# Performance work log

Measured on AMD Instinct MI355X. Metric: run time of the kernel, lower is better.

Reference implementation:

```python
import jax, jax.numpy as jnp
import numpy as np


def _conv_bn_relu(x, w, g, b):
    # 1x1 conv over channel dim + BatchNorm(eval, affine) + ReLU; x: [B,Cin,...]
    y = jnp.einsum('oc,bc...->bo...', w, x)
    shp = (1, -1) + (1,) * (y.ndim - 2)
    return jax.nn.relu(y * g.reshape(shp) + b.reshape(shp))


def _gather(feat, idx):
    # feat [B,d,N], idx [B,M] -> [B,d,M]  (torch.gather along dim 2)
    return jnp.take_along_axis(feat, idx[:, None, :], axis=2)


def _lfa(f, neigh_idx, w, g, b):
    # Local Feature Aggregation: gather k neighbors, concat with center, 1x1 conv, max over k.
    Bn, Np, k = neigh_idx.shape
    fs = f[..., 0]                                   # [B,d,N]
    d = fs.shape[1]
    neigh = _gather(fs, neigh_idx.reshape(Bn, Np * k)).reshape(Bn, d, Np, k)
    cat = jnp.concatenate([jnp.broadcast_to(f, neigh.shape), neigh], axis=1)  # [B,2d,N,k]
    return _conv_bn_relu(cat, w, g, b).max(axis=3, keepdims=True)             # [B,d_out,N,1]


def _random_sample(f, pool_idx):
    # f [B,d,N,1], pool_idx [B,N',k] -> [B,d,N',1] via gather + max over k
    Bn, Np, k = pool_idx.shape
    fs = f[..., 0]
    d = fs.shape[1]
    gth = _gather(fs, pool_idx.reshape(Bn, Np * k)).reshape(Bn, d, Np, k)
    return gth.max(axis=3, keepdims=True)


def _interp(f, interp_idx):
    # f [B,d,N,1], interp_idx [B,M,1] -> [B,d,M,1] nearest-neighbor upsample
    Bn, M, _ = interp_idx.shape
    return _gather(f[..., 0], interp_idx.reshape(Bn, M))[..., None]


def setup_inputs() -> dict:
    key = jax.random.key(0)
    B, K = 2, 16
    Ns = (16384, 4096, 1024, 256, 64)
    ks = list(jax.random.split(key, 64))
    ki = iter(ks)
    inp = {}
    inp['xyz'] = jax.random.normal(next(ki), (B, Ns[0], 3), jnp.float32)
    for i in range(4):
        inp['neigh%d' % i] = jax.random.randint(next(ki), (B, Ns[i], K), 0, Ns[i], jnp.int32)
        inp['pool%d' % i] = jax.random.randint(next(ki), (B, Ns[i + 1], K), 0, Ns[i], jnp.int32)
        inp['up%d' % i] = jax.random.randint(next(ki), (B, Ns[i], 1), 0, Ns[i + 1], jnp.int32)

    def mk(name, co, cin):
        inp[name + '_w'] = jax.random.normal(next(ki), (co, cin), jnp.float32) * 0.02
        inp[name + '_g'] = jnp.ones((co,), jnp.float32)
        inp[name + '_b'] = jnp.zeros((co,), jnp.float32)

    mk('fc0', 64, 3)
    mk('l1', 128, 128)
    mk('l2', 256, 256)
    mk('l3', 512, 512)
    mk('l4', 1024, 1024)
    mk('dt', 1024, 1024)
    mk('d4', 512, 2048)
    mk('d3', 256, 1024)
    mk('d2', 128, 512)
    mk('d1', 64, 256)
    mk('d0', 64, 64)
    return inp


def reference(xyz, neigh0, neigh1, neigh2, neigh3, pool0, pool1, pool2, pool3, up0, up1, up2, up3, fc0_w, fc0_g, fc0_b, l1_w, l1_g, l1_b, l2_w, l2_g, l2_b, l3_w, l3_g, l3_b, l4_w, l4_g, l4_b, dt_w, dt_g, dt_b, d4_w, d4_g, d4_b, d3_w, d3_g, d3_b, d2_w, d2_g, d2_b, d1_w, d1_g, d1_b, d0_w, d0_g, d0_b):
    out0 = _conv_bn_relu(jnp.transpose(xyz, (0, 2, 1)), fc0_w, fc0_g, fc0_b)[..., None]  # [B,64,N0,1]
    out1 = _lfa(out0, neigh0, l1_w, l1_g, l1_b)        # [B,128,N0,1]
    out1p = _random_sample(out1, pool0)                # [B,128,N1,1]
    out2 = _lfa(out1p, neigh1, l2_w, l2_g, l2_b)       # [B,256,N1,1]
    out2p = _random_sample(out2, pool1)                # [B,256,N2,1]
    out3 = _lfa(out2p, neigh2, l3_w, l3_g, l3_b)       # [B,512,N2,1]
    out3p = _random_sample(out3, pool2)                # [B,512,N3,1]
    out4 = _lfa(out3p, neigh3, l4_w, l4_g, l4_b)       # [B,1024,N3,1]
    out4p = _random_sample(out4, pool3)                # [B,1024,N4,1]
    out = _conv_bn_relu(out4p, dt_w, dt_g, dt_b)
    out = _conv_bn_relu(jnp.concatenate([out, out4p], 1), d4_w, d4_g, d4_b)
    out = _interp(out, up3)
    out = _conv_bn_relu(jnp.concatenate([out, out3p], 1), d3_w, d3_g, d3_b)
    out = _interp(out, up2)
    out = _conv_bn_relu(jnp.concatenate([out, out2p], 1), d2_w, d2_g, d2_b)
    out = _interp(out, up1)
    out = _conv_bn_relu(jnp.concatenate([out, out1p], 1), d1_w, d1_g, d1_b)
    out = _interp(out, up0)
    out = _conv_bn_relu(out, d0_w, d0_g, d0_b)         # [B,out_d,N0,1]
    return out
```

## Files before the change

### kernel.cpp

```cpp
#include <hip/hip_runtime.h>

typedef unsigned short u16;
typedef unsigned int u32;
typedef short s16x8 __attribute__((ext_vector_type(8)));
typedef float f32x4 __attribute__((ext_vector_type(4)));

__device__ __forceinline__ float bf2f(u16 u) {
  union { u32 i; float f; } c;
  c.i = ((u32)u) << 16;
  return c.f;
}
__device__ __forceinline__ u16 f2bf(float f) {
  union { float f; u32 i; } c;
  c.f = f;
  u32 r = c.i + 0x7FFFu + ((c.i >> 16) & 1u);
  return (u16)(r >> 16);
}
__device__ __forceinline__ float rbf(float x) {
  union { float f; u32 u; } c;
  c.f = x;
  u32 r = c.u + 0x7FFFu + ((c.u >> 16) & 1u);
  c.u = (r >> 16) << 16;
  return c.f;
}
__device__ __forceinline__ float ldin(const void* p, size_t i, int isBf) {
  if (isBf) return bf2f(((const u16*)p)[i]);
  return rbf(((const float*)p)[i]);
}
__device__ __forceinline__ void ld4bf(const u16* p, float* v) {
  uint2 q = *reinterpret_cast<const uint2*>(p);
  v[0] = bf2f((u16)(q.x & 0xFFFFu));
  v[1] = bf2f((u16)(q.x >> 16));
  v[2] = bf2f((u16)(q.y & 0xFFFFu));
  v[3] = bf2f((u16)(q.y >> 16));
}
__device__ __forceinline__ void st4bf(u16* p, const float* v) {
  uint2 q;
  q.x = (u32)f2bf(v[0]) | (((u32)f2bf(v[1])) << 16);
  q.y = (u32)f2bf(v[2]) | (((u32)f2bf(v[3])) << 16);
  *reinterpret_cast<uint2*>(p) = q;
}

__global__ void C3Dnet_34600256537193_kernel() {}

__global__ void probe_kernel(const u16* x, int* flag) {
  if (threadIdx.x == 0 && blockIdx.x == 0) {
    int sane = 0;
    for (int i = 0; i < 256; i += 2) {
      int e = (x[i] >> 7) & 0xFF;
      if (e >= 97 && e <= 137) ++sane;
    }
    *flag = (sane >= 64) ? 1 : 0;
  }
}

__global__ __launch_bounds__(256) void sentinel_kernel(u16* out, int n, float v) {
  u16 u = f2bf(v);
  int i0 = (blockIdx.x * 256 + threadIdx.x) * 8;
  for (int j = 0; j < 8; ++j)
    if (i0 + j < n) out[i0 + j] = u;
}

__global__ __launch_bounds__(256) void cvt_kernel(
    const void* s0, const void* s1, const void* s2, const void* s3, const void* s4,
    const void* s5, const void* s6, const void* s7, const void* s8, const void* s9,
    u16* dst, const int* dtF) {
  const int f = *dtF;
  int blk = blockIdx.x;
  const void* src;
  int base, boff;
  if (blk < 8)         { src = s0; base = 0;       boff = 0;    }
  else if (blk < 40)   { src = s1; base = 16384;   boff = 8;    }
  else if (blk < 168)  { src = s2; base = 81920;   boff = 40;   }
  else if (blk < 680)  { src = s3; base = 344064;  boff = 168;  }
  else if (blk < 1192) { src = s4; base = 1392640; boff = 680;  }
  else if (blk < 1704) { src = s5; base = 2441216; boff = 1192; }
  else if (blk < 1832) { src = s6; base = 3489792; boff = 1704; }
  else if (blk < 1864) { src = s7; base = 3751936; boff = 1832; }
  else if (blk < 1872) { src = s8; base = 3817472; boff = 1864; }
  else                 { src = s9; base = 3833856; boff = 1872; }
  int local = (blk - boff) * 2048 + (int)threadIdx.x * 8;
  u16* dp = dst + base + local;
  if (f) {
    *reinterpret_cast<uint4*>(dp) =
        *reinterpret_cast<const uint4*>((const u16*)src + local);
  } else {
    const float4* sp = reinterpret_cast<const float4*>((const float*)src + local);
    float4 a = sp[0], b = sp[1];
    uint4 o;
    o.x = (u32)f2bf(a.x) | (((u32)f2bf(a.y)) << 16);
    o.y = (u32)f2bf(a.z) | (((u32)f2bf(a.w)) << 16);
    o.z = (u32)f2bf(b.x) | (((u32)f2bf(b.y)) << 16);
    o.w = (u32)f2bf(b.z) | (((u32)f2bf(b.w)) << 16);
    *reinterpret_cast<uint4*>(dp) = o;
  }
}

__global__ __launch_bounds__(256) void fc0_kernel(
    const void* xyz, const void* w, const void* g, const void* be,
    u16* out, int N, const int* dtF) {
  int f = *dtF;
  int o = threadIdx.x & 63;
  int n = blockIdx.x * 4 + (threadIdx.x >> 6);
  int b = blockIdx.y;
  if (n >= N) return;
  size_t pb = ((size_t)b * N + n) * 3;
  float acc = ldin(w, o * 3 + 0, f) * ldin(xyz, pb + 0, f) +
              ldin(w, o * 3 + 1, f) * ldin(xyz, pb + 1, f) +
              ldin(w, o * 3 + 2, f) * ldin(xyz, pb + 2, f);
  acc = acc * ldin(g, o, f) + ldin(be, o, f);
  if (acc < 0.0f) acc = 0.0f;
  out[((size_t)b * N + n) * 64 + o] = f2bf(acc);
}

__global__ __launch_bounds__(256) void gather_max_kernel(
    const void* src, int srcBf16, int srcStride, int srcOff, int Nsrc,
    const void* cen, int cenBf16, int cenStride,
    const int* idx, void* out, int outBf16, int Np, int C, int doRelu) {
  int c4n = C >> 2;
  int ptsPerBlk = 256 / c4n;
  int p = (int)threadIdx.x / c4n;
  int c4 = (int)threadIdx.x % c4n;
  int n = blockIdx.x * ptsPerBlk + p;
  int b = blockIdx.y;
  if (n >= Np) return;
  const int* ip = idx + ((size_t)b * Np + n) * 16;
  float m[4];
  m[0] = m[1] = m[2] = m[3] = -3.0e38f;
  for (int k = 0; k < 16; ++k) {
    size_t base = ((size_t)b * Nsrc + ip[k]) * srcStride + srcOff + (c4 << 2);
    float v[4];
    if (srcBf16) {
      ld4bf((const u16*)src + base, v);
    } else {
      float4 t = *reinterpret_cast<const float4*>((const float*)src + base);
      v[0] = t.x; v[1] = t.y; v[2] = t.z; v[3] = t.w;
    }
    for (int j = 0; j < 4; ++j)
      if (v[j] > m[j]) m[j] = v[j];
  }
  if (cen) {
    size_t cb = ((size_t)b * Np + n) * cenStride + (c4 << 2);
    float cv[4];
    if (cenBf16) {
      ld4bf((const u16*)cen + cb, cv);
    } else {
      float4 t = *reinterpret_cast<const float4*>((const float*)cen + cb);
      cv[0] = t.x; cv[1] = t.y; cv[2] = t.z; cv[3] = t.w;
    }
    for (int j = 0; j < 4; ++j) m[j] += cv[j];
  }
  if (doRelu) {
    for (int j = 0; j < 4; ++j)
      if (m[j] < 0.0f) m[j] = 0.0f;
  }
  size_t ob = ((size_t)b * Np + n) * C + (c4 << 2);
  if (outBf16) {
    st4bf((u16*)out + ob, m);
  } else {
    float4 t;
    t.x = m[0]; t.y = m[1]; t.z = m[2]; t.w = m[3];
    *reinterpret_cast<float4*>((float*)out + ob) = t;
  }
}

__global__ __launch_bounds__(256) void gather_max8_kernel(
    const u16* src, int srcStride, int srcOff, int Nsrc,
    const u16* cen, int cenStride,
    const int* idx, void* out, int outBf16, int Np, int C, int doRelu) {
  int c8n = C >> 3;
  int ptsPerBlk = 256 / c8n;
  int p = (int)threadIdx.x / c8n;
  int c8 = (int)threadIdx.x % c8n;
  int n = blockIdx.x * ptsPerBlk + p;
  int b = blockIdx.y;
  if (n >= Np) return;
  const int* ip = idx + ((size_t)b * Np + n) * 16;
  float m[8];
  #pragma unroll
  for (int j = 0; j < 8; ++j) m[j] = -3.0e38f;
  for (int k = 0; k < 16; ++k) {
    const u16* sp = src + ((size_t)b * Nsrc + ip[k]) * srcStride + srcOff + (c8 << 3);
    uint4 q = *reinterpret_cast<const uint4*>(sp);
    float v[8];
    v[0] = bf2f((u16)(q.x & 0xFFFFu)); v[1] = bf2f((u16)(q.x >> 16));
    v[2] = bf2f((u16)(q.y & 0xFFFFu)); v[3] = bf2f((u16)(q.y >> 16));
    v[4] = bf2f((u16)(q.z & 0xFFFFu)); v[5] = bf2f((u16)(q.z >> 16));
    v[6] = bf2f((u16)(q.w & 0xFFFFu)); v[7] = bf2f((u16)(q.w >> 16));
    #pragma unroll
    for (int j = 0; j < 8; ++j)
      if (v[j] > m[j]) m[j] = v[j];
  }
  if (cen) {
    const u16* cp = cen + ((size_t)b * Np + n) * cenStride + (c8 << 3);
    uint4 q = *reinterpret_cast<const uint4*>(cp);
    m[0] += bf2f((u16)(q.x & 0xFFFFu)); m[1] += bf2f((u16)(q.x >> 16));
    m[2] += bf2f((u16)(q.y & 0xFFFFu)); m[3] += bf2f((u16)(q.y >> 16));
    m[4] += bf2f((u16)(q.z & 0xFFFFu)); m[5] += bf2f((u16)(q.z >> 16));
    m[6] += bf2f((u16)(q.w & 0xFFFFu)); m[7] += bf2f((u16)(q.w >> 16));
  }
  if (doRelu) {
    #pragma unroll
    for (int j = 0; j < 8; ++j)
      if (m[j] < 0.0f) m[j] = 0.0f;
  }
  size_t ob = ((size_t)b * Np + n) * C + (c8 << 3);
  if (outBf16) {
    uint4 q;
    q.x = (u32)f2bf(m[0]) | (((u32)f2bf(m[1])) << 16);
    q.y = (u32)f2bf(m[2]) | (((u32)f2bf(m[3])) << 16);
    q.z = (u32)f2bf(m[4]) | (((u32)f2bf(m[5])) << 16);
    q.w = (u32)f2bf(m[6]) | (((u32)f2bf(m[7])) << 16);
    *reinterpret_cast<uint4*>((u16*)out + ob) = q;
  } else {
    float4 t0, t1;
    t0.x = m[0]; t0.y = m[1]; t0.z = m[2]; t0.w = m[3];
    t1.x = m[4]; t1.y = m[5]; t1.z = m[6]; t1.w = m[7];
    *reinterpret_cast<float4*>((float*)out + ob) = t0;
    *reinterpret_cast<float4*>((float*)out + ob + 4) = t1;
  }
}

__global__ __launch_bounds__(256) void mfma_gemm_kernel(
    const u16* W, int wld,
    const u16* X, int cin, int Nn,
    const void* gamma, const void* beta,
    void* out, int outBf16,
    int OD, int odHalf, int doRelu, const int* dtF) {
  __shared__ u16 Ws[128 * 40];
  const int f = *dtF;
  const int b = blockIdx.z;
  const int n0 = blockIdx.x * 64;
  const int o0 = blockIdx.y * 128;
  const int tid = threadIdx.x;
  const int wid = tid >> 6;
  const int lane = tid & 63;
  const int lr = lane & 15;
  const int lq = lane >> 4;

  f32x4 acc0 = {0.f,0.f,0.f,0.f}, acc1 = acc0, acc2 = acc0, acc3 = acc0;
  f32x4 acc4 = acc0, acc5 = acc0, acc6 = acc0, acc7 = acc0;

  const u16* xp = X + ((size_t)b * Nn + (n0 + wid * 16 + lr)) * cin + lq * 8;

  for (int kk = 0; kk < cin; kk += 32) {
    for (int i = 0; i < 2; ++i) {
      int idx = tid + i * 256;
      int row = idx >> 2, q = idx & 3;
      int o = o0 + row;
      int wr = o, ko = 0;
      if (odHalf && o >= odHalf) { wr = o - odHalf; ko = cin; }
      *reinterpret_cast<uint4*>(&Ws[row * 40 + q * 8]) =
          *reinterpret_cast<const uint4*>(W + (size_t)wr * wld + ko + kk + q * 8);
    }
    __syncthreads();
    s16x8 a = *reinterpret_cast<const s16x8*>(xp + kk);
    s16x8 b0 = *reinterpret_cast<const s16x8*>(&Ws[(0 * 16 + lr) * 40 + lq * 8]);
    acc0 = __builtin_amdgcn_mfma_f32_16x16x32_bf16(a, b0, acc0, 0, 0, 0);
    s16x8 b1 = *reinterpret_cast<const s16x8*>(&Ws[(1 * 16 + lr) * 40 + lq * 8]);
    acc1 = __builtin_amdgcn_mfma_f32_16x16x32_bf16(a, b1, acc1, 0, 0, 0);
    s16x8 b2 = *reinterpret_cast<const s16x8*>(&Ws[(2 * 16 + lr) * 40 + lq * 8]);
    acc2 = __builtin_amdgcn_mfma_f32_16x16x32_bf16(a, b2, acc2, 0, 0, 0);
    s16x8 b3 = *reinterpret_cast<const s16x8*>(&Ws[(3 * 16 + lr) * 40 + lq * 8]);
    acc3 = __builtin_amdgcn_mfma_f32_16x16x32_bf16(a, b3, acc3, 0, 0, 0);
    s16x8 b4 = *reinterpret_cast<const s16x8*>(&Ws[(4 * 16 + lr) * 40 + lq * 8]);
    acc4 = __builtin_amdgcn_mfma_f32_16x16x32_bf16(a, b4, acc4, 0, 0, 0);
    s16x8 b5 = *reinterpret_cast<const s16x8*>(&Ws[(5 * 16 + lr) * 40 + lq * 8]);
    acc5 = __builtin_amdgcn_mfma_f32_16x16x32_bf16(a, b5, acc5, 0, 0, 0);
    s16x8 b6 = *reinterpret_cast<const s16x8*>(&Ws[(6 * 16 + lr) * 40 + lq * 8]);
    acc6 = __builtin_amdgcn_mfma_f32_16x16x32_bf16(a, b6, acc6, 0, 0, 0);
    s16x8 b7 = *reinterpret_cast<const s16x8*>(&Ws[(7 * 16 + lr) * 40 + lq * 8]);
    acc7 = __builtin_amdgcn_mfma_f32_16x16x32_bf16(a, b7, acc7, 0, 0, 0);
    __syncthreads();
  }

  f32x4 av[8] = {acc0, acc1, acc2, acc3, acc4, acc5, acc6, acc7};
  #pragma unroll
  for (int ot = 0; ot < 8; ++ot) {
    int o = o0 + ot * 16 + lr;
    int og = (odHalf && o >= odHalf) ? (o - odHalf) : o;
    float ga = ldin(gamma, og, f);
    float bb = (!odHalf || o < odHalf) ? ldin(beta, og, f) : 0.0f;
    #pragma unroll
    for (int r = 0; r < 4; ++r) {
      int n = n0 + wid * 16 + lq * 4 + r;
      float x = av[ot][r] * ga + bb;
      if (doRelu && x < 0.0f) x = 0.0f;
      size_t oi = ((size_t)b * Nn + n) * OD + o;
      if (outBf16) ((u16*)out)[oi] = f2bf(x);
      else ((float*)out)[oi] = x;
    }
  }
}

#define DEF_SGEMV(KNAME, P)                                                        \
__global__ __launch_bounds__(256) void KNAME(                                      \
    const u16* Wc, const void* Wraw, int useCvt, int wld,                          \
    const float* X1, int cin1, int n1src,                                          \
    const float* X2, int cin2, int x2bf,                                           \
    const int* map1,                                                               \
    const void* gamma, const void* beta,                                           \
    float* out,                                                                    \
    int N, int OD, int odHalf, int doRelu, const int* dtF, int nf4Log) {           \
  extern __shared__ float xrow[];                                                  \
  const int f = *dtF;                                                              \
  const int b = blockIdx.y;                                                        \
  const int odt = OD >> 6;                                                         \
  const int ng = (int)blockIdx.x / odt;                                            \
  const int o0 = ((int)blockIdx.x % odt) * 64;                                     \
  const int n0 = ng * P;                                                           \
  const int nf4 = 1 << nf4Log;                                                     \
  const int cin = nf4 << 2;                                                        \
  const int tid = threadIdx.x;                                                     \
  for (int idx4 = tid; idx4 < (P * cin) >> 2; idx4 += 256) {                       \
    int p = idx4 >> nf4Log;                                                        \
    int c = (idx4 & (nf4 - 1)) << 2;                                               \
    int n = n0 + p;                                                                \
    float v4[4];                                                                   \
    if (c < cin1) {                                                                \
      int rs = map1 ? map1[(size_t)b * N + n] : n;                                 \
      float4 v = *reinterpret_cast<const float4*>(X1 + ((size_t)b * n1src + rs) * cin1 + c); \
      v4[0] = v.x; v4[1] = v.y; v4[2] = v.z; v4[3] = v.w;                          \
    } else {                                                                       \
      size_t xo = ((size_t)b * N + n) * cin2 + (c - cin1);                         \
      if (x2bf) {                                                                  \
        ld4bf((const u16*)(const void*)X2 + xo, v4);                               \
      } else {                                                                     \
        float4 v = *reinterpret_cast<const float4*>(X2 + xo);                      \
        v4[0] = v.x; v4[1] = v.y; v4[2] = v.z; v4[3] = v.w;                        \
      }                                                                            \
    }                                                                              \
    xrow[(p << (nf4Log + 2)) + c + 0] = v4[0];                                     \
    xrow[(p << (nf4Log + 2)) + c + 1] = v4[1];                                     \
    xrow[(p << (nf4Log + 2)) + c + 2] = v4[2];                                     \
    xrow[(p << (nf4Log + 2)) + c + 3] = v4[3];                                     \
  }                                                                                \
  __syncthreads();                                                                 \
  const int o = o0 + (tid >> 2);                                                   \
  const int q = tid & 3;                                                           \
  int wr = o, wo = 0, useBeta = 1;                                                 \
  if (odHalf && o >= odHalf) { wr = o - odHalf; wo = cin1; useBeta = 0; }          \
  float sums[P];                                                                   \
  _Pragma("unroll") for (int p = 0; p < P; ++p) sums[p] = 0.0f;                    \
  if (useCvt) {                                                                    \
    const u16* wp = Wc + (size_t)wr * wld + wo;                                    \
    for (int i = q; i < nf4; i += 4) {                                             \
      float wv[4];                                                                 \
      ld4bf(wp + (i << 2), wv);                                                    \
      _Pragma("unroll") for (int p = 0; p < P; ++p) {                              \
        const float4 xv = *reinterpret_cast<const float4*>(                        \
            &xrow[(p << (nf4Log + 2)) + (i << 2)]);                                \
        sums[p] += wv[0] * xv.x + wv[1] * xv.y + wv[2] * xv.z + wv[3] * xv.w;      \
      }                                                                            \
    }                                                                              \
  } else if (f) {                                                                  \
    const u16* wp = (const u16*)Wraw + (size_t)wr * wld + wo;                      \
    for (int i = q; i < nf4; i += 4) {                                             \
      float wv[4];                                                                 \
      ld4bf(wp + (i << 2), wv);                                                    \
      _Pragma("unroll") for (int p = 0; p < P; ++p) {                              \
        const float4 xv = *reinterpret_cast<const float4*>(                        \
            &xrow[(p << (nf4Log + 2)) + (i << 2)]);                                \
        sums[p] += wv[0] * xv.x + wv[1] * xv.y + wv[2] * xv.z + wv[3] * xv.w;      \
      }                                                                            \
    }                                                                              \
  } else {                                                                         \
    const float* wp = (const float*)Wraw + (size_t)wr * wld + wo;                  \
    for (int i = q; i < nf4; i += 4) {                                             \
      float4 wv = *reinterpret_cast<const float4*>(wp + (i << 2));                 \
      float w0 = rbf(wv.x), w1 = rbf(wv.y), w2 = rbf(wv.z), w3 = rbf(wv.w);        \
      _Pragma("unroll") for (int p = 0; p < P; ++p) {                              \
        const float4 xv = *reinterpret_cast<const float4*>(                        \
            &xrow[(p << (nf4Log + 2)) + (i << 2)]);                                \
        sums[p] += w0 * xv.x + w1 * xv.y + w2 * xv.z + w3 * xv.w;                  \
      }                                                                            \
    }                                                                              \
  }                                                                                \
  _Pragma("unroll") for (int p = 0; p < P; ++p) {                                  \
    sums[p] += __shfl_xor(sums[p], 1);                                             \
    sums[p] += __shfl_xor(sums[p], 2);                                             \
  }                                                                                \
  int og = (odHalf && o >= odHalf) ? (o - odHalf) : o;                             \
  float ga = ldin(gamma, og, f);                                                   \
  float bb = useBeta ? ldin(beta, og, f) : 0.0f;                                   \
  _Pragma("unroll") for (int pp = 0; pp < P / 4; ++pp) {                           \
    int p = q * (P / 4) + pp;                                                      \
    float x = sums[p] * ga + bb;                                                   \
    if (doRelu && x < 0.0f) x = 0.0f;                                              \
    out[((size_t)b * N + (n0 + p)) * OD + o] = x;                                  \
  }                                                                                \
}

DEF_SGEMV(sgemv_p4, 4)
DEF_SGEMV(sgemv_p8, 8)
DEF_SGEMV(sgemv_p16, 16)

#define GTK 16
#define LSTR 68
__global__ __launch_bounds__(256) void gemm_kernel(
    const u16* Wc, const void* Wraw, int useCvt, int wld,
    const void* X1, int x1bf16, int cin1, int n1src,
    const float* X2, int cin2,
    const int* map1,
    const void* gamma, const void* beta,
    void* out, int outMode,
    int N, int OD, int odHalf, int doRelu, const int* dtF) {
  __shared__ float XsT[GTK * LSTR];
  __shared__ float WsT[GTK * LSTR];
  const int f = *dtF;
  const int b = blockIdx.z;
  const int n0 = blockIdx.x * 64;
  const int o0 = blockIdx.y * 64;
  const int tid = threadIdx.x;
  const int tx = tid & 15;
  const int ty = tid >> 4;
  const int cin = cin1 + cin2;
  float acc[4][4];
  for (int i = 0; i < 4; ++i)
    for (int j = 0; j < 4; ++j) acc[i][j] = 0.0f;

  for (int kk = 0; kk < cin; kk += GTK) {
    for (int l = 0; l < 4; ++l) {
      int e = tid + l * 256;
      int r = e >> 4, c = e & 15;
      int cc = kk + c;
      int n = n0 + r;
      float v = 0.0f;
      if (cc < cin) {
        if (cc < cin1) {
          int rs = map1 ? map1[(size_t)b * N + n] : n;
          size_t xi = ((size_t)b * n1src + rs) * cin1 + cc;
          v = x1bf16 ? bf2f(((const u16*)X1)[xi]) : ((const float*)X1)[xi];
        } else {
          v = X2[((size_t)b * N + n) * cin2 + (cc - cin1)];
        }
      }
      XsT[c * LSTR + r] = v;
    }
    for (int l = 0; l < 4; ++l) {
      int e = tid + l * 256;
      int r = e >> 4, c = e & 15;
      int o = o0 + r, cc = kk + c;
      float v = 0.0f;
      if (cc < cin) {
        int wr = o, wo = 0;
        if (odHalf && o >= odHalf) { wr = o - odHalf; wo = cin1; }
        size_t wi = (size_t)wr * wld + wo + cc;
        v = useCvt ? bf2f(Wc[wi]) : ldin(Wraw, wi, f);
      }
      WsT[c * LSTR + r] = v;
    }
    __syncthreads();
    #pragma unroll
    for (int c = 0; c < GTK; ++c) {
      float a4[4], w4[4];
      *reinterpret_cast<float4*>(a4) =
          *reinterpret_cast<const float4*>(&XsT[c * LSTR + ty * 4]);
      *reinterpret_cast<float4*>(w4) =
          *reinterpret_cast<const float4*>(&WsT[c * LSTR + tx * 4]);
      for (int i = 0; i < 4; ++i)
        for (int j = 0; j < 4; ++j) acc[i][j] += a4[i] * w4[j];
    }
    __syncthreads();
  }

  if (outMode == 2) {
    for (int j = 0; j < 4; ++j) {
      int o = o0 + tx * 4 + j;
      float ga = ldin(gamma, o, f), bb = ldin(beta, o, f);
      float x4[4];
      for (int i = 0; i < 4; ++i) {
        float x = acc[i][j] * ga + bb;
        if (doRelu && x < 0.0f) x = 0.0f;
        x4[i] = x;
      }
      size_t po = ((size_t)b * OD + o) * N + n0 + ty * 4;
      if (f) {
        uint2 q;
        q.x = (u32)f2bf(x4[0]) | (((u32)f2bf(x4[1])) << 16);
        q.y = (u32)f2bf(x4[2]) | (((u32)f2bf(x4[3])) << 16);
        *reinterpret_cast<uint2*>((u16*)out + po) = q;
      } else {
        float4 t;
        t.x = x4[0]; t.y = x4[1]; t.z = x4[2]; t.w = x4[3];
        *reinterpret_cast<float4*>((float*)out + po) = t;
      }
    }
  } else {
    for (int i = 0; i < 4; ++i) {
      int n = n0 + ty * 4 + i;
      float vv[4];
      for (int j = 0; j < 4; ++j) {
        int o = o0 + tx * 4 + j;
        float x = acc[i][j];
        int og = (odHalf && o >= odHalf) ? (o - odHalf) : o;
        x *= ldin(gamma, og, f);
        if (!odHalf || o < odHalf) x += ldin(beta, og, f);
        if (doRelu && x < 0.0f) x = 0.0f;
        vv[j] = x;
      }
      size_t ob = ((size_t)b * N + n) * OD + o0 + tx * 4;
      if (outMode == 1) {
        st4bf((u16*)out + ob, vv);
      } else {
        float4 t;
        t.x = vv[0]; t.y = vv[1]; t.z = vv[2]; t.w = vv[3];
        *reinterpret_cast<float4*>((float*)out + ob) = t;
      }
    }
  }
}

extern "C" void kernel_launch(void* const* d_in, const int* in_sizes, int n_in,
                              void* d_out, int out_size, void* d_ws, size_t ws_size,
                              hipStream_t stream) {
  (void)in_sizes;
  (void)n_in;
  const int B = 2;
  const int N0 = 16384, N1 = 4096, N2 = 1024, N3 = 256, N4 = 64;
  const int* nb0 = (const int*)d_in[1];
  const int* pl0 = (const int*)d_in[2];
  const int* up0 = (const int*)d_in[3];
  const int* nb1 = (const int*)d_in[4];
  const int* pl1 = (const int*)d_in[5];
  const int* up1 = (const int*)d_in[6];
  const int* nb2 = (const int*)d_in[7];
  const int* pl2 = (const int*)d_in[8];
  const int* up2 = (const int*)d_in[9];
  const int* nb3 = (const int*)d_in[10];
  const int* pl3 = (const int*)d_in[11];
  const int* up3 = (const int*)d_in[12];

  {
    float v = 1000.0f + 4.0f * (float)(ws_size >> 20);
    int nblk = (out_size + 2047) / 2048;
    sentinel_kernel<<<dim3(nblk), dim3(256), 0, stream>>>((u16*)d_out, out_size, v);
  }

  float* ws = (float*)d_ws;
  u16* out1p = (u16*)(ws + 0);
  u16* out2p = (u16*)(ws + 1048576);
  float* out3p = ws + 1572864;
  float* out4p = ws + 1835008;
  const size_t TZ = 1966080;
  u16* cpgp1 = (u16*)(ws + TZ);
  u16* out0 = (u16*)(ws + TZ + 4194304);
  u16* out1 = (u16*)(ws + TZ + 4194304);
  u16* cpgp2 = (u16*)(ws + TZ);
  float* out2 = ws + TZ + 2097152;
  float* cpgp3 = ws + TZ;
  float* out3 = ws + TZ + 2097152;
  float* cpgp4 = ws + TZ;
  float* out4 = ws + TZ + 1048576;
  float* dto = ws + TZ;
  float* d4o = ws + TZ + 131072;
  float* d3o = ws + TZ + 196608;
  float* d2o = ws + TZ + 327680;
  float* d1o = ws + TZ + 589824;
  int* dtF = (int*)(ws + TZ + 6291456);
  u16* wcvt = (u16*)(ws + TZ + 6291456 + 8);

  const size_t NEED_MIN = (TZ + 6291456 + 4) * sizeof(float);
  const size_t NEED_BIG = (TZ + 6291456 + 8 + 1918976) * sizeof(float);
  if (d_ws == 0 || ws_size < NEED_MIN) return;
  const int CVT = (ws_size >= NEED_BIG) ? 1 : 0;

  u16* w_l1 = wcvt + 0;
  u16* w_l2 = wcvt + 16384;
  u16* w_l3 = wcvt + 81920;
  u16* w_l4 = wcvt + 344064;
  u16* w_dt = wcvt + 1392640;
  u16* w_d4 = wcvt + 2441216;
  u16* w_d3 = wcvt + 3489792;
  u16* w_d2 = wcvt + 3751936;
  u16* w_d1 = wcvt + 3817472;
  u16* w_d0 = wcvt + 3833856;

  probe_kernel<<<dim3(1), dim3(64), 0, stream>>>((const u16*)d_in[0], dtF);
  if (CVT) {
    cvt_kernel<<<dim3(1874), dim3(256), 0, stream>>>(
        d_in[16], d_in[19], d_in[22], d_in[25], d_in[28],
        d_in[31], d_in[34], d_in[37], d_in[40], d_in[43], wcvt, dtF);
  }

  fc0_kernel<<<dim3(N0 / 4, B), dim3(256), 0, stream>>>(
      d_in[0], d_in[13], d_in[14], d_in[15], out0, N0, dtF);

  if (CVT) {
    mfma_gemm_kernel<<<dim3(N0 / 64, 256 / 128, B), dim3(256), 0, stream>>>(
        w_l1, 128, out0, 64, N0, d_in[17], d_in[18], cpgp1, 1, 256, 128, 0, dtF);
  } else {
    gemm_kernel<<<dim3(N0 / 64, 256 / 64, B), dim3(256), 0, stream>>>(
        w_l1, d_in[16], CVT, 128, out0, 1, 64, N0, (const float*)0, 0, (const int*)0,
        d_in[17], d_in[18], cpgp1, 1, N0, 256, 128, 0, dtF);
  }
  gather_max8_kernel<<<dim3(N0 / 16, B), dim3(256), 0, stream>>>(
      cpgp1, 256, 128, N0, cpgp1, 256, nb0, out1, 1, N0, 128, 1);
  gather_max8_kernel<<<dim3(N1 / 16, B), dim3(256), 0, stream>>>(
      out1, 128, 0, N0, (const u16*)0, 0, pl0, out1p, 1, N1, 128, 0);

  if (CVT) {
    mfma_gemm_kernel<<<dim3(N1 / 64, 512 / 128, B), dim3(256), 0, stream>>>(
        w_l2, 256, out1p, 128, N1, d_in[20], d_in[21], cpgp2, 1, 512, 256, 0, dtF);
  } else {
    gemm_kernel<<<dim3(N1 / 64, 512 / 64, B), dim3(256), 0, stream>>>(
        w_l2, d_in[19], CVT, 256, out1p, 1, 128, N1, (const float*)0, 0, (const int*)0,
        d_in[20], d_in[21], cpgp2, 1, N1, 512, 256, 0, dtF);
  }
  gather_max8_kernel<<<dim3(N1 / 8, B), dim3(256), 0, stream>>>(
      cpgp2, 512, 256, N1, cpgp2, 512, nb1, out2, 0, N1, 256, 1);
  gather_max_kernel<<<dim3(N2 / 4, B), dim3(256), 0, stream>>>(
      out2, 0, 256, 0, N1, (const void*)0, 0, 0, pl1, out2p, 1, N2, 256, 0);

  if (CVT) {
    mfma_gemm_kernel<<<dim3(N2 / 64, 1024 / 128, B), dim3(256), 0, stream>>>(
        w_l3, 512, out2p, 256, N2, d_in[23], d_in[24], cpgp3, 0, 1024, 512, 0, dtF);
  } else {
    gemm_kernel<<<dim3(N2 / 64, 1024 / 64, B), dim3(256), 0, stream>>>(
        w_l3, d_in[22], CVT, 512, out2p, 1, 256, N2, (const float*)0, 0, (const int*)0,
        d_in[23], d_in[24], cpgp3, 0, N2, 1024, 512, 0, dtF);
  }
  gather_max_kernel<<<dim3(N2 / 2, B), dim3(256), 0, stream>>>(
      cpgp3, 0, 1024, 512, N2, cpgp3, 0, 1024, nb2, out3, 0, N2, 512, 1);
  gather_max_kernel<<<dim3(N3 / 2, B), dim3(256), 0, stream>>>(
      out3, 0, 512, 0, N2, (const void*)0, 0, 0, pl2, out3p, CVT, N3, 512, 0);

  if (CVT) {
    mfma_gemm_kernel<<<dim3(N3 / 64, 2048 / 128, B), dim3(256), 0, stream>>>(
        w_l4, 1024, (const u16*)(void*)out3p, 512, N3, d_in[26], d_in[27],
        cpgp4, 0, 2048, 1024, 0, dtF);
  } else {
    sgemv_p16<<<dim3((N3 / 16) * (2048 / 64), B), dim3(256), 32768, stream>>>(
        w_l4, d_in[25], CVT, 1024, out3p, 512, N3, (const float*)0, 0, 0, (const int*)0,
        d_in[26], d_in[27], cpgp4, N3, 2048, 1024, 0, dtF, 7);
  }
  gather_max_kernel<<<dim3(N3, B), dim3(256), 0, stream>>>(
      cpgp4, 0, 2048, 1024, N3, cpgp4, 0, 2048, nb3, out4, 0, N3, 1024, 1);
  gather_max_kernel<<<dim3(N4, B), dim3(256), 0, stream>>>(
      out4, 0, 1024, 0, N3, (const void*)0, 0, 0, pl3, out4p, 0, N4, 1024, 0);

  sgemv_p8<<<dim3((N4 / 8) * (1024 / 64), B), dim3(256), 32768, stream>>>(
      w_dt, d_in[28], CVT, 1024, out4p, 1024, N4, (const float*)0, 0, 0, (const int*)0,
      d_in[29], d_in[30], dto, N4, 1024, 0, 1, dtF, 8);
  sgemv_p4<<<dim3((N4 / 4) * (512 / 64), B), dim3(256), 32768, stream>>>(
      w_d4, d_in[31], CVT, 2048, dto, 1024, N4, out4p, 1024, 0, (const int*)0,
      d_in[32], d_in[33], d4o, N4, 512, 0, 1, dtF, 9);
  sgemv_p8<<<dim3((N3 / 8) * (256 / 64), B), dim3(256), 32768, stream>>>(
      w_d3, d_in[34], CVT, 1024, d4o, 512, N4, out3p, 512, CVT, up3,
      d_in[35], d_in[36], d3o, N3, 256, 0, 1, dtF, 8);
  sgemv_p16<<<dim3((N2 / 16) * (128 / 64), B), dim3(256), 32768, stream>>>(
      w_d2, d_in[37], CVT, 512, d3o, 256, N3, (const float*)(void*)out2p, 256, 1, up2,
      d_in[38], d_in[39], d2o, N2, 128, 0, 1, dtF, 7);
  sgemv_p16<<<dim3((N1 / 16) * (64 / 64), B), dim3(256), 16384, stream>>>(
      w_d1, d_in[40], CVT, 256, d2o, 128, N2, (const float*)(void*)out1p, 128, 1, up1,
      d_in[41], d_in[42], d1o, N1, 64, 0, 1, dtF, 6);
  gemm_kernel<<<dim3(N0 / 64, 64 / 64, B), dim3(256), 0, stream>>>(
      w_d0, d_in[43], CVT, 64, d1o, 0, 64, N1, (const float*)0, 0, up0,
      d_in[44], d_in[45], d_out, 2, N0, 64, 0, 1, dtF);
}
```

Before: 302.7 us.

## Split CVT path, fold dtype probe into cvt, use bf16 intermediates for layers 2-3

Splits the host launch sequence into a dedicated CVT branch and a fallback branch. The dtype probe kernel is folded into cvt_kernel, and the sentinel fill now runs only on the error path, which removes two launches from the normal flow. In the CVT path, layers 2 and 3 write bf16 intermediates and use the gather_max8 kernels instead of the fp32 gather_max, cutting memory traffic. The trade-offs are extra probe work in every cvt block and possible small precision differences from the bf16 intermediates.

```diff
diff --git a/kernel.cpp b/kernel.cpp
--- a/kernel.cpp
+++ b/kernel.cpp
@@ -40,18 +40,19 @@
   q.y = (u32)f2bf(v[2]) | (((u32)f2bf(v[3])) << 16);
   *reinterpret_cast<uint2*>(p) = q;
 }
+__device__ __forceinline__ int probe_dtype(const u16* x) {
+  int sane = 0;
+  for (int i = 0; i < 256; i += 2) {
+    int e = (x[i] >> 7) & 0xFF;
+    if (e >= 97 && e <= 137) ++sane;
+  }
+  return (sane >= 64) ? 1 : 0;
+}
 
 __global__ void C3Dnet_34600256537193_kernel() {}
 
 __global__ void probe_kernel(const u16* x, int* flag) {
-  if (threadIdx.x == 0 && blockIdx.x == 0) {
-    int sane = 0;
-    for (int i = 0; i < 256; i += 2) {
-      int e = (x[i] >> 7) & 0xFF;
-      if (e >= 97 && e <= 137) ++sane;
-    }
-    *flag = (sane >= 64) ? 1 : 0;
-  }
+  if (threadIdx.x == 0 && blockIdx.x == 0) *flag = probe_dtype(x);
 }
 
 __global__ __launch_bounds__(256) void sentinel_kernel(u16* out, int n, float v) {
@@ -64,8 +65,15 @@
 __global__ __launch_bounds__(256) void cvt_kernel(
     const void* s0, const void* s1, const void* s2, const void* s3, const void* s4,
     const void* s5, const void* s6, const void* s7, const void* s8, const void* s9,
-    u16* dst, const int* dtF) {
-  const int f = *dtF;
+    u16* dst, const u16* xyz, int* dtF) {
+  __shared__ int fsh;
+  if (threadIdx.x == 0) {
+    int f0 = probe_dtype(xyz);
+    fsh = f0;
+    if (blockIdx.x == 0) *dtF = f0;
+  }
+  __syncthreads();
+  const int f = fsh;
   int blk = blockIdx.x;
   const void* src;
   int base, boff;
@@ -301,7 +309,7 @@
     const int* map1,                                                               \
     const void* gamma, const void* beta,                                           \
     float* out,                                                                    \
-    int N, int OD, int odHalf, int doRelu, const int* dtF, int nf4Log) {           \
+    int N, int OD, int odHalf, int doRelu, const int* dtF, int nf4Log, int outBf) {\
   extern __shared__ float xrow[];                                                  \
   const int f = *dtF;                                                              \
   const int b = blockIdx.y;                                                        \
@@ -387,7 +395,9 @@
     int p = q * (P / 4) + pp;                                                      \
     float x = sums[p] * ga + bb;                                                   \
     if (doRelu && x < 0.0f) x = 0.0f;                                              \
-    out[((size_t)b * N + (n0 + p)) * OD + o] = x;                                  \
+    size_t oi = ((size_t)b * N + (n0 + p)) * OD + o;                               \
+    if (outBf) ((u16*)(void*)out)[oi] = f2bf(x);                                   \
+    else out[oi] = x;                                                              \
   }                                                                                \
 }
 
@@ -531,12 +541,6 @@
   const int* pl3 = (const int*)d_in[11];
   const int* up3 = (const int*)d_in[12];
 
-  {
-    float v = 1000.0f + 4.0f * (float)(ws_size >> 20);
-    int nblk = (out_size + 2047) / 2048;
-    sentinel_kernel<<<dim3(nblk), dim3(256), 0, stream>>>((u16*)d_out, out_size, v);
-  }
-
   float* ws = (float*)d_ws;
   u16* out1p = (u16*)(ws + 0);
   u16* out2p = (u16*)(ws + 1048576);
@@ -562,7 +566,12 @@
 
   const size_t NEED_MIN = (TZ + 6291456 + 4) * sizeof(float);
   const size_t NEED_BIG = (TZ + 6291456 + 8 + 1918976) * sizeof(float);
-  if (d_ws == 0 || ws_size < NEED_MIN) return;
+  if (d_ws == 0 || ws_size < NEED_MIN) {
+    float v = 1000.0f + 4.0f * (float)(ws_size >> 20);
+    int nblk = (out_size + 2047) / 2048;
+    sentinel_kernel<<<dim3(nblk), dim3(256), 0, stream>>>((u16*)d_out, out_size, v);
+    return;
+  }
   const int CVT = (ws_size >= NEED_BIG) ? 1 : 0;
 
   u16* w_l1 = wcvt + 0;
@@ -576,85 +585,112 @@
   u16* w_d1 = wcvt + 3817472;
   u16* w_d0 = wcvt + 3833856;
 
-  probe_kernel<<<dim3(1), dim3(64), 0, stream>>>((const u16*)d_in[0], dtF);
   if (CVT) {
     cvt_kernel<<<dim3(1874), dim3(256), 0, stream>>>(
         d_in[16], d_in[19], d_in[22], d_in[25], d_in[28],
-        d_in[31], d_in[34], d_in[37], d_in[40], d_in[43], wcvt, dtF);
-  }
-
+        d_in[31], d_in[34], d_in[37], d_in[40], d_in[43],
+        wcvt, (const u16*)d_in[0], dtF);
+
+    fc0_kernel<<<dim3(N0 / 4, B), dim3(256), 0, stream>>>(
+        d_in[0], d_in[13], d_in[14], d_in[15], out0, N0, dtF);
+    mfma_gemm_kernel<<<dim3(N0 / 64, 256 / 128, B), dim3(256), 0, stream>>>(
+        w_l1, 128, out0, 64, N0, d_in[17], d_in[18], cpgp1, 1, 256, 128, 0, dtF);
+    gather_max8_kernel<<<dim3(N0 / 16, B), dim3(256), 0, stream>>>(
+        cpgp1, 256, 128, N0, cpgp1, 256, nb0, out1, 1, N0, 128, 1);
+    gather_max8_kernel<<<dim3(N1 / 16, B), dim3(256), 0, stream>>>(
+        out1, 128, 0, N0, (const u16*)0, 0, pl0, out1p, 1, N1, 128, 0);
+
+    mfma_gemm_kernel<<<dim3(N1 / 64, 512 / 128, B), dim3(256), 0, stream>>>(
+        w_l2, 256, out1p, 128, N1, d_in[20], d_in[21], cpgp2, 1, 512, 256, 0, dtF);
+    gather_max8_kernel<<<dim3(N1 / 8, B), dim3(256), 0, stream>>>(
+        cpgp2, 512, 256, N1, cpgp2, 512, nb1, out2, 1, N1, 256, 1);
+    gather_max8_kernel<<<dim3(N2 / 8, B), dim3(256), 0, stream>>>(
+        (const u16*)(void*)out2, 256, 0, N1, (const u16*)0, 0, pl1, out2p, 1, N2, 256, 0);
+
+    mfma_gemm_kernel<<<dim3(N2 / 64, 1024 / 128, B), dim3(256), 0, stream>>>(
+        w_l3, 512, out2p, 256, N2, d_in[23], d_in[24], cpgp3, 1, 1024, 512, 0, dtF);
+    gather_max8_kernel<<<dim3(N2 / 4, B), dim3(256), 0, stream>>>(
+        (const u16*)(void*)cpgp3, 1024, 512, N2, (const u16*)(void*)cpgp3, 1024,
+        nb2, out3, 1, N2, 512, 1);
+    gather_max8_kernel<<<dim3(N3 / 4, B), dim3(256), 0, stream>>>(
+        (const u16*)(void*)out3, 512, 0, N2, (const u16*)0, 0, pl2, out3p, 1, N3, 512, 0);
+
+    mfma_gemm_kernel<<<dim3(N3 / 64, 2048 / 128, B), dim3(256), 0, stream>>>(
+        w_l4, 1024, (const u16*)(void*)out3p, 512, N3, d_in[26], d_in[27],
+        cpgp4, 0, 2048, 1024, 0, dtF);
+    gather_max_kernel<<<dim3(N3, B), dim3(256), 0, stream>>>(
+        cpgp4, 0, 2048, 1024, N3, cpgp4, 0, 2048, nb3, out4, 0, N3, 1024, 1);
+    gather_max_kernel<<<dim3(N4, B), dim3(256), 0, stream>>>(
+        out4, 0, 1024, 0, N3, (const void*)0, 0, 0, pl3, out4p, 0, N4, 1024, 0);
+
+    sgemv_p8<<<dim3((N4 / 8) * (1024 / 64), B), dim3(256), 32768, stream>>>(
+        w_dt, d_in[28], 1, 1024, out4p, 1024, N4, (const float*)0, 0, 0, (const int*)0,
+        d_in[29], d_in[30], dto, N4, 1024, 0, 1, dtF, 8, 0);
+    sgemv_p4<<<dim3((N4 / 4) * (512 / 64), B), dim3(256), 32768, stream>>>(
+        w_d4, d_in[31], 1, 2048, dto, 1024, N4, out4p, 1024, 0, (const int*)0,
+        d_in[32], d_in[33], d4o, N4, 512, 0, 1, dtF, 9, 0);
+    sgemv_p8<<<dim3((N3 / 8) * (256 / 64), B), dim3(256), 32768, stream>>>(
+        w_d3, d_in[34], 1, 1024, d4o, 512, N4, out3p, 512, 1, up3,
+        d_in[35], d_in[36], d3o, N3, 256, 0, 1, dtF, 8, 0);
+    sgemv_p16<<<dim3((N2 / 16) * (128 / 64), B), dim3(256), 32768, stream>>>(
+        w_d2, d_in[37], 1, 512, d3o, 256, N3, (const float*)(void*)out2p, 256, 1, up2,
+        d_in[38], d_in[39], d2o, N2, 128, 0, 1, dtF, 7, 0);
+    sgemv_p16<<<dim3((N1 / 16) * (64 / 64), B), dim3(256), 16384, stream>>>(
+        w_d1, d_in[40], 1, 256, d2o, 128, N2, (const float*)(void*)out1p, 128, 1, up1,
+        d_in[41], d_in[42], d1o, N1, 64, 0, 1, dtF, 6, 0);
+    gemm_kernel<<<dim3(N0 / 64, 64 / 64, B), dim3(256), 0, stream>>>(
+        w_d0, d_in[43], 1, 64, d1o, 0, 64, N1, (const float*)0, 0, up0,
+        d_in[44], d_in[45], d_out, 2, N0, 64, 0, 1, dtF);
+    return;
+  }
+
+  probe_kernel<<<dim3(1), dim3(64), 0, stream>>>((const u16*)d_in[0], dtF);
   fc0_kernel<<<dim3(N0 / 4, B), dim3(256), 0, stream>>>(
       d_in[0], d_in[13], d_in[14], d_in[15], out0, N0, dtF);
-
-  if (CVT) {
-    mfma_gemm_kernel<<<dim3(N0 / 64, 256 / 128, B), dim3(256), 0, stream>>>(
-        w_l1, 128, out0, 64, N0, d_in[17], d_in[18], cpgp1, 1, 256, 128, 0, dtF);
-  } else {
-    gemm_kernel<<<dim3(N0 / 64, 256 / 64, B), dim3(256), 0, stream>>>(
-        w_l1, d_in[16], CVT, 128, out0, 1, 64, N0, (const float*)0, 0, (const int*)0,
-        d_in[17], d_in[18], cpgp1, 1, N0, 256, 128, 0, dtF);
-  }
+  gemm_kernel<<<dim3(N0 / 64, 256 / 64, B), dim3(256), 0, stream>>>(
+      w_l1, d_in[16], 0, 128, out0, 1, 64, N0, (const float*)0, 0, (const int*)0,
+      d_in[17], d_in[18], cpgp1, 1, N0, 256, 128, 0, dtF);
   gather_max8_kernel<<<dim3(N0 / 16, B), dim3(256), 0, stream>>>(
       cpgp1, 256, 128, N0, cpgp1, 256, nb0, out1, 1, N0, 128, 1);
   gather_max8_kernel<<<dim3(N1 / 16, B), dim3(256), 0, stream>>>(
       out1, 128, 0, N0, (const u16*)0, 0, pl0, out1p, 1, N1, 128, 0);
-
-  if (CVT) {
-    mfma_gemm_kernel<<<dim3(N1 / 64, 512 / 128, B), dim3(256), 0, stream>>>(
-        w_l2, 256, out1p, 128, N1, d_in[20], d_in[21], cpgp2, 1, 512, 256, 0, dtF);
-  } else {
-    gemm_kernel<<<dim3(N1 / 64, 512 / 64, B), dim3(256), 0, stream>>>(
-        w_l2, d_in[19], CVT, 256, out1p, 1, 128, N1, (const float*)0, 0, (const int*)0,
-        d_in[20], d_in[21], cpgp2, 1, N1, 512, 256, 0, dtF);
-  }
+  gemm_kernel<<<dim3(N1 / 64, 512 / 64, B), dim3(256), 0, stream>>>(
+      w_l2, d_in[19], 0, 256, out1p, 1, 128, N1, (const float*)0, 0, (const int*)0,
+      d_in[20], d_in[21], cpgp2, 1, N1, 512, 256, 0, dtF);
   gather_max8_kernel<<<dim3(N1 / 8, B), dim3(256), 0, stream>>>(
       cpgp2, 512, 256, N1, cpgp2, 512, nb1, out2, 0, N1, 256, 1);
   gather_max_kernel<<<dim3(N2 / 4, B), dim3(256), 0, stream>>>(
       out2, 0, 256, 0, N1, (const void*)0, 0, 0, pl1, out2p, 1, N2, 256, 0);
-
-  if (CVT) {
-    mfma_gemm_kernel<<<dim3(N2 / 64, 1024 / 128, B), dim3(256), 0, stream>>>(
-        w_l3, 512, out2p, 256, N2, d_in[23], d_in[24], cpgp3, 0, 1024, 512, 0, dtF);
-  } else {
-    gemm_kernel<<<dim3(N2 / 64, 1024 / 64, B), dim3(256), 0, stream>>>(
-        w_l3, d_in[22], CVT, 512, out2p, 1, 256, N2, (const float*)0, 0, (const int*)0,
-        d_in[23], d_in[24], cpgp3, 0, N2, 1024, 512, 0, dtF);
-  }
+  gemm_kernel<<<dim3(N2 / 64, 1024 / 64, B), dim3(256), 0, stream>>>(
+      w_l3, d_in[22], 0, 512, out2p, 1, 256, N2, (const float*)0, 0, (const int*)0,
+      d_in[23], d_in[24], cpgp3, 0, N2, 1024, 512, 0, dtF);
   gather_max_kernel<<<dim3(N2 / 2, B), dim3(256), 0, stream>>>(
       cpgp3, 0, 1024, 512, N2, cpgp3, 0, 1024, nb2, out3, 0, N2, 512, 1);
   gather_max_kernel<<<dim3(N3 / 2, B), dim3(256), 0, stream>>>(
-      out3, 0, 512, 0, N2, (const void*)0, 0, 0, pl2, out3p, CVT, N3, 512, 0);
-
-  if (CVT) {
-    mfma_gemm_kernel<<<dim3(N3 / 64, 2048 / 128, B), dim3(256), 0, stream>>>(
-        w_l4, 1024, (const u16*)(void*)out3p, 512, N3, d_in[26], d_in[27],
-        cpgp4, 0, 2048, 1024, 0, dtF);
-  } else {
-    sgemv_p16<<<dim3((N3 / 16) * (2048 / 64), B), dim3(256), 32768, stream>>>(
-        w_l4, d_in[25], CVT, 1024, out3p, 512, N3, (const float*)0, 0, 0, (const int*)0,
-        d_in[26], d_in[27], cpgp4, N3, 2048, 1024, 0, dtF, 7);
-  }
+      out3, 0, 512, 0, N2, (const void*)0, 0, 0, pl2, out3p, 0, N3, 512, 0);
+  sgemv_p16<<<dim3((N3 / 16) * (2048 / 64), B), dim3(256), 32768, stream>>>(
+      w_l4, d_in[25], 0, 1024, out3p, 512, N3, (const float*)0, 0, 0, (const int*)0,
+      d_in[26], d_in[27], cpgp4, N3, 2048, 1024, 0, dtF, 7, 0);
   gather_max_kernel<<<dim3(N3, B), dim3(256), 0, stream>>>(
       cpgp4, 0, 2048, 1024, N3, cpgp4, 0, 2048, nb3, out4, 0, N3, 1024, 1);
   gather_max_kernel<<<dim3(N4, B), dim3(256), 0, stream>>>(
       out4, 0, 1024, 0, N3, (const void*)0, 0, 0, pl3, out4p, 0, N4, 1024, 0);
-
   sgemv_p8<<<dim3((N4 / 8) * (1024 / 64), B), dim3(256), 32768, stream>>>(
-      w_dt, d_in[28], CVT, 1024, out4p, 1024, N4, (const float*)0, 0, 0, (const int*)0,
-      d_in[29], d_in[30], dto, N4, 1024, 0, 1, dtF, 8);
+      w_dt, d_in[28], 0, 1024, out4p, 1024, N4, (const float*)0, 0, 0, (const int*)0,
+      d_in[29], d_in[30], dto, N4, 1024, 0, 1, dtF, 8, 0);
   sgemv_p4<<<dim3((N4 / 4) * (512 / 64), B), dim3(256), 32768, stream>>>(
-      w_d4, d_in[31], CVT, 2048, dto, 1024, N4, out4p, 1024, 0, (const int*)0,
-      d_in[32], d_in[33], d4o, N4, 512, 0, 1, dtF, 9);
+      w_d4, d_in[31], 0, 2048, dto, 1024, N4, out4p, 1024, 0, (const int*)0,
+      d_in[32], d_in[33], d4o, N4, 512, 0, 1, dtF, 9, 0);
   sgemv_p8<<<dim3((N3 / 8) * (256 / 64), B), dim3(256), 32768, stream>>>(
-      w_d3, d_in[34], CVT, 1024, d4o, 512, N4, out3p, 512, CVT, up3,
-      d_in[35], d_in[36], d3o, N3, 256, 0, 1, dtF, 8);
+      w_d3, d_in[34], 0, 1024, d4o, 512, N4, out3p, 512, 0, up3,
+      d_in[35], d_in[36], d3o, N3, 256, 0, 1, dtF, 8, 0);
   sgemv_p16<<<dim3((N2 / 16) * (128 / 64), B), dim3(256), 32768, stream>>>(
-      w_d2, d_in[37], CVT, 512, d3o, 256, N3, (const float*)(void*)out2p, 256, 1, up2,
-      d_in[38], d_in[39], d2o, N2, 128, 0, 1, dtF, 7);
+      w_d2, d_in[37], 0, 512, d3o, 256, N3, (const float*)(void*)out2p, 256, 1, up2,
+      d_in[38], d_in[39], d2o, N2, 128, 0, 1, dtF, 7, 0);
   sgemv_p16<<<dim3((N1 / 16) * (64 / 64), B), dim3(256), 16384, stream>>>(
-      w_d1, d_in[40], CVT, 256, d2o, 128, N2, (const float*)(void*)out1p, 128, 1, up1,
-      d_in[41], d_in[42], d1o, N1, 64, 0, 1, dtF, 6);
+      w_d1, d_in[40], 0, 256, d2o, 128, N2, (const float*)(void*)out1p, 128, 1, up1,
+      d_in[41], d_in[42], d1o, N1, 64, 0, 1, dtF, 6, 0);
   gemm_kernel<<<dim3(N0 / 64, 64 / 64, B), dim3(256), 0, stream>>>(
-      w_d0, d_in[43], CVT, 64, d1o, 0, 64, N1, (const float*)0, 0, up0,
+      w_d0, d_in[43], 0, 64, d1o, 0, 64, N1, (const float*)0, 0, up0,
       d_in[44], d_in[45], d_out, 2, N0, 64, 0, 1, dtF);
 }
```

Measured after the change: 301.6 us. No clear change (-0.4%).
